# Performance work log

Measured on AMD Instinct MI355X. Metric: run time of the kernel, lower is better.

The kernel has to match this reference:

```python
import jax, jax.numpy as jnp
import numpy as np

BETA = 0.25


def setup_inputs() -> dict:
    key = jax.random.key(0)
    k1, k2 = jax.random.split(key)
    z = jax.random.normal(k1, (16, 64, 64, 64), dtype=jnp.float32)        # [B, e_dim, H, W]
    codebook = jax.random.normal(k2, (2048, 64), dtype=jnp.float32)       # [n_e, e_dim]
    return {"z": z, "codebook": codebook}


def reference(z, codebook):
    B, C, H, W = z.shape
    n_e = codebook.shape[0]
    sg = jax.lax.stop_gradient

    zp = jnp.transpose(z, (0, 2, 3, 1))                # [B, H, W, C]
    zf = zp.reshape(-1, C)                             # [N, C]

    # nearest-code logits (inner product; CE in source is dead code)
    logits = zf @ codebook.T                           # [N, n_e]
    idx = jnp.argmax(logits, axis=1)                   # [N]

    z_q = codebook[idx].reshape(zp.shape)              # [B, H, W, C]

    # commitment + codebook loss (this overwrites the CE loss in the source)
    loss = BETA * jnp.mean((sg(z_q) - zp) ** 2) + jnp.mean((z_q - sg(zp)) ** 2)

    # straight-through estimator
    z_q_st = zp + sg(z_q - zp)

    # perplexity via one-hot mean (scatter-add instead of dense one-hot)
    counts = jnp.zeros((n_e,), dtype=zp.dtype).at[idx].add(1.0)
    e_mean = counts / idx.shape[0]
    perplexity = jnp.exp(-jnp.sum(e_mean * jnp.log(e_mean + 1e-10)))

    indices = idx.reshape(B, H * W).astype(jnp.int32)
    z_q_out = jnp.transpose(z_q_st, (0, 3, 1, 2))      # back to [B, C, H, W]
    return z_q_out, loss, perplexity, indices
```

## Files before the change

### kernel.cpp

```cpp
#include <hip/hip_runtime.h>

#define C_DIM   64
#define HW      4096
#define NROWS   65536
#define N_E     2048
#define N_ELEM  4194304
#define OUT_LOSS_OFF 4194304
#define OUT_PPL_OFF  4194305
#define OUT_IDX_OFF  4194306

#define ROWS_B   128
#define NBLOCKS  (NROWS / ROWS_B)
#define NTILE    (N_E / 16)
#define TILE_U   384

typedef __attribute__((ext_vector_type(8))) short bf16x8;
typedef __attribute__((ext_vector_type(4))) float f32x4;

__device__ __forceinline__ unsigned short f2bf(float f) {
    unsigned u = __float_as_uint(f);
    return (unsigned short)((u + 0x7FFFu + ((u >> 16) & 1u)) >> 16);
}
__device__ __forceinline__ float bf2f(unsigned short b) {
    return __uint_as_float(((unsigned)b) << 16);
}

__global__ __launch_bounds__(256) void vq_prep(
    const float* __restrict__ cb, unsigned short* __restrict__ cbp,
    int* __restrict__ counts, float* __restrict__ loss_accum,
    int* __restrict__ done)
{
    const int u = blockIdx.x * 256 + threadIdx.x;
    if (u < N_E) counts[u] = 0;
    if (u == 0)  { *loss_accum = 0.f; *done = 0; }

    const int lane = u & 63;
    const int k2   = (u >> 6) & 1;
    const int tile = u >> 7;
    const int c    = tile * 16 + (lane & 15);
    const int k0   = k2 * 32 + (lane >> 4) * 8;

    const float4 va = *(const float4*)(cb + (size_t)c * C_DIM + k0);
    const float4 vb = *(const float4*)(cb + (size_t)c * C_DIM + k0 + 4);
    const float v[8] = {va.x, va.y, va.z, va.w, vb.x, vb.y, vb.z, vb.w};

    bf16x8 s1v, s2v, s3v;
#pragma unroll
    for (int i = 0; i < 8; ++i) {
        const unsigned short s1 = f2bf(v[i]);
        const float r1 = v[i] - bf2f(s1);
        const unsigned short s2 = f2bf(r1);
        const float r2 = r1 - bf2f(s2);
        s1v[i] = (short)s1;
        s2v[i] = (short)s2;
        s3v[i] = (short)f2bf(r2);
    }
    const size_t base = ((size_t)(tile * 3 + 0) * 2 + k2) * 512 + (size_t)lane * 8;
    *(bf16x8*)(cbp + base)        = s1v;
    *(bf16x8*)(cbp + base + 1024) = s2v;
    *(bf16x8*)(cbp + base + 2048) = s3v;
}

#define M16(A_, B_, C_) __builtin_amdgcn_mfma_f32_16x16x32_bf16((A_), (B_), (C_), 0, 0, 0)

#define PASS8(AA, ACC, NT)                                                      \
    ACC = M16(AA[0], zf[0][NT][0], ACC); ACC = M16(AA[1], zf[0][NT][1], ACC);   \
    ACC = M16(AA[0], zf[1][NT][0], ACC); ACC = M16(AA[1], zf[1][NT][1], ACC);   \
    ACC = M16(AA[2], zf[0][NT][0], ACC); ACC = M16(AA[3], zf[0][NT][1], ACC);   \
    ACC = M16(AA[2], zf[1][NT][0], ACC); ACC = M16(AA[3], zf[1][NT][1], ACC);   \
    ACC = M16(AA[0], zf[2][NT][0], ACC); ACC = M16(AA[1], zf[2][NT][1], ACC);   \
    ACC = M16(AA[4], zf[0][NT][0], ACC); ACC = M16(AA[5], zf[0][NT][1], ACC);   \
    ACC = M16(AA[2], zf[2][NT][0], ACC); ACC = M16(AA[3], zf[2][NT][1], ACC);   \
    ACC = M16(AA[4], zf[1][NT][0], ACC); ACC = M16(AA[5], zf[1][NT][1], ACC);

#define COMPUTE_TILE(T_, AA)                                                    \
    {                                                                           \
        f32x4 acc0 = zero4, acc1 = zero4;                                       \
        PASS8(AA, acc0, 0)                                                      \
        PASS8(AA, acc1, 1)                                                      \
        const int cbase = (T_) * 16 + lg * 4;                                   \
        _Pragma("unroll")                                                       \
        for (int r = 0; r < 4; ++r) {                                           \
            if (acc0[r] > best0) { best0 = acc0[r]; bi0 = cbase + r; }          \
            if (acc1[r] > best1) { best1 = acc1[r]; bi1 = cbase + r; }          \
        }                                                                       \
    }

#define LOADA(AA, T_)                                                           \
    {                                                                           \
        const bf16x8* p_ = cbpf + (size_t)(T_) * TILE_U;                        \
        _Pragma("unroll")                                                       \
        for (int f = 0; f < 6; ++f) AA[f] = p_[f * 64 + lane];                  \
    }

__global__ __launch_bounds__(256, 2) void vq_mfma(
    const float* __restrict__ z, const float* __restrict__ cb,
    const unsigned short* __restrict__ cbp, float* __restrict__ out,
    int* __restrict__ counts, float* __restrict__ loss_accum,
    int* __restrict__ done)
{
    __shared__ int   sidx[ROWS_B];
    __shared__ float wsum[4];
    __shared__ int   slast;

    const int tid  = threadIdx.x;
    const int lane = tid & 63;
    const int wv   = tid >> 6;
    const int l15  = lane & 15, lg = lane >> 4;
    const int row0 = blockIdx.x * ROWS_B;
    const int b    = row0 >> 12;
    const int hw0  = row0 & 4095;
    const float* zb = z + (size_t)b * C_DIM * HW + hw0;

    if (tid == 0) slast = 0;

    bf16x8 zf[3][2][2];
#pragma unroll
    for (int nt = 0; nt < 2; ++nt) {
        const int row_l = wv * 32 + nt * 16 + l15;
#pragma unroll
        for (int k2 = 0; k2 < 2; ++k2) {
#pragma unroll
            for (int i = 0; i < 8; ++i) {
                float v = zb[(size_t)(k2 * 32 + lg * 8 + i) * HW + row_l];
                unsigned short s1 = f2bf(v);
                float r1 = v - bf2f(s1);
                unsigned short s2 = f2bf(r1);
                float r2 = r1 - bf2f(s2);
                zf[0][nt][k2][i] = (short)s1;
                zf[1][nt][k2][i] = (short)s2;
                zf[2][nt][k2][i] = (short)f2bf(r2);
            }
        }
    }

    const bf16x8* cbpf = (const bf16x8*)cbp;
    float best0 = -3.4e38f, best1 = -3.4e38f;
    int   bi0 = 0, bi1 = 0;
    const f32x4 zero4 = {0.f, 0.f, 0.f, 0.f};

    bf16x8 A0[6], A1[6], A2[6], A3[6];
    LOADA(A0, 0) LOADA(A1, 1) LOADA(A2, 2)

#pragma unroll 1
    for (int t = 0; t < NTILE; t += 4) {
        const int p3 = t + 3;
        const int p4 = (t + 4 < NTILE) ? t + 4 : NTILE - 1;
        const int p5 = (t + 5 < NTILE) ? t + 5 : NTILE - 1;
        const int p6 = (t + 6 < NTILE) ? t + 6 : NTILE - 1;
        LOADA(A3, p3) COMPUTE_TILE(t,     A0)
        LOADA(A0, p4) COMPUTE_TILE(t + 1, A1)
        LOADA(A1, p5) COMPUTE_TILE(t + 2, A2)
        LOADA(A2, p6) COMPUTE_TILE(t + 3, A3)
    }

#pragma unroll
    for (int off = 16; off <= 32; off <<= 1) {
        float ob; int oi;
        ob = __shfl_xor(best0, off, 64); oi = __shfl_xor(bi0, off, 64);
        if (ob > best0 || (ob == best0 && oi < bi0)) { best0 = ob; bi0 = oi; }
        ob = __shfl_xor(best1, off, 64); oi = __shfl_xor(bi1, off, 64);
        if (ob > best1 || (ob == best1 && oi < bi1)) { best1 = ob; bi1 = oi; }
    }
    if (lane < 32) {
        const int nt = lane >> 4;
        const int row_l = wv * 32 + lane;
        const int ii = (nt == 0) ? bi0 : bi1;
        sidx[row_l] = ii;
        out[OUT_IDX_OFF + row0 + row_l] = (float)ii;
        atomicAdd(&counts[ii], 1);
    }
    __syncthreads();

    float* ob0 = out + (size_t)b * C_DIM * HW + hw0;
    float lsum = 0.f;
#pragma unroll
    for (int j = 0; j < 8; ++j) {
        const int m = j * 256 + tid;
        const int r = m & 127, c4 = m >> 7;
        const float4 q4 = *(const float4*)(cb + (size_t)sidx[r] * C_DIM + c4 * 4);
#pragma unroll
        for (int q = 0; q < 4; ++q) {
            const int c = c4 * 4 + q;
            const float zv = zb[(size_t)c * HW + r];
            const float qv = (q == 0) ? q4.x : (q == 1) ? q4.y : (q == 2) ? q4.z : q4.w;
            const float d = qv - zv;
            lsum += d * d;
            ob0[(size_t)c * HW + r] = zv + d;
        }
    }
    for (int off = 32; off > 0; off >>= 1) lsum += __shfl_down(lsum, off, 64);
    if (lane == 0) wsum[wv] = lsum;
    __syncthreads();

    if (tid == 0) {
        atomicAdd(loss_accum, wsum[0] + wsum[1] + wsum[2] + wsum[3]);
        __threadfence();
        const int tk = atomicAdd(done, 1);
        if (tk == NBLOCKS - 1) slast = 1;
    }
    __syncthreads();
    if (slast) {
        __threadfence();
        float h = 0.f;
        for (int e = tid; e < N_E; e += 256) {
            const int cnt = atomicAdd(&counts[e], 0);
            const float em = (float)cnt * (1.0f / (float)NROWS);
            h -= em * logf(em + 1e-10f);
        }
        for (int off = 32; off > 0; off >>= 1) h += __shfl_down(h, off, 64);
        if (lane == 0) wsum[wv] = h;
        __syncthreads();
        if (tid == 0) {
            const float H = wsum[0] + wsum[1] + wsum[2] + wsum[3];
            const float L = atomicAdd(loss_accum, 0.f);
            const float m = L * (1.0f / (float)N_ELEM);
            out[OUT_LOSS_OFF] = 0.25f * m + m;
            out[OUT_PPL_OFF]  = expf(H);
        }
    }
}

extern "C" void kernel_launch(void* const* d_in, const int* in_sizes, int n_in,
                              void* d_out, int out_size, void* d_ws, size_t ws_size,
                              hipStream_t stream)
{
    const float* z  = (const float*)d_in[0];
    const float* cb = (const float*)d_in[1];
    float* out = (float*)d_out;

    int*            counts     = (int*)d_ws;
    float*          loss_accum = (float*)((char*)d_ws + N_E * sizeof(int));
    int*            done       = (int*)((char*)d_ws + N_E * sizeof(int) + 4);
    unsigned short* cbp        = (unsigned short*)((char*)d_ws + 16384);

    vq_prep<<<64, 256, 0, stream>>>(cb, cbp, counts, loss_accum, done);
    vq_mfma<<<NBLOCKS, 256, 0, stream>>>(z, cb, cbp, out, counts, loss_accum, done);
}
```

Baseline: 188.1 us.

## Fuse codebook bf16 split into main kernel and replace prep kernel with memset

Removes the separate prep kernel that pre-split the codebook into three bf16 parts. The main kernel now loads raw fp32 codebook rows and does the three-way bf16 split inline, one tile ahead, with double buffering of raw loads instead of a four-deep prefetch of split fragments. Counters are zeroed with a memset. This drops one launch and the packed codebook traffic, but every block now repeats the split ALU work for all 2048 codes, which adds VALU work to the MFMA loop, and the prefetch distance is shorter.

New measurement: 242.2 us. 1.29x slower.

```diff
diff --git a/kernel.cpp b/kernel.cpp
--- a/kernel.cpp
+++ b/kernel.cpp
@@ -12,7 +12,6 @@
 #define ROWS_B   128
 #define NBLOCKS  (NROWS / ROWS_B)
 #define NTILE    (N_E / 16)
-#define TILE_U   384
 
 typedef __attribute__((ext_vector_type(8))) short bf16x8;
 typedef __attribute__((ext_vector_type(4))) float f32x4;
@@ -25,40 +24,22 @@
     return __uint_as_float(((unsigned)b) << 16);
 }
 
-__global__ __launch_bounds__(256) void vq_prep(
-    const float* __restrict__ cb, unsigned short* __restrict__ cbp,
-    int* __restrict__ counts, float* __restrict__ loss_accum,
-    int* __restrict__ done)
+__device__ __forceinline__ void split8(const float4 a, const float4 b,
+                                       bf16x8* s1v, bf16x8* s2v, bf16x8* s3v)
 {
-    const int u = blockIdx.x * 256 + threadIdx.x;
-    if (u < N_E) counts[u] = 0;
-    if (u == 0)  { *loss_accum = 0.f; *done = 0; }
-
-    const int lane = u & 63;
-    const int k2   = (u >> 6) & 1;
-    const int tile = u >> 7;
-    const int c    = tile * 16 + (lane & 15);
-    const int k0   = k2 * 32 + (lane >> 4) * 8;
-
-    const float4 va = *(const float4*)(cb + (size_t)c * C_DIM + k0);
-    const float4 vb = *(const float4*)(cb + (size_t)c * C_DIM + k0 + 4);
-    const float v[8] = {va.x, va.y, va.z, va.w, vb.x, vb.y, vb.z, vb.w};
-
-    bf16x8 s1v, s2v, s3v;
+    const float v[8] = {a.x, a.y, a.z, a.w, b.x, b.y, b.z, b.w};
+    bf16x8 t1, t2, t3;
 #pragma unroll
     for (int i = 0; i < 8; ++i) {
         const unsigned short s1 = f2bf(v[i]);
         const float r1 = v[i] - bf2f(s1);
         const unsigned short s2 = f2bf(r1);
         const float r2 = r1 - bf2f(s2);
-        s1v[i] = (short)s1;
-        s2v[i] = (short)s2;
-        s3v[i] = (short)f2bf(r2);
-    }
-    const size_t base = ((size_t)(tile * 3 + 0) * 2 + k2) * 512 + (size_t)lane * 8;
-    *(bf16x8*)(cbp + base)        = s1v;
-    *(bf16x8*)(cbp + base + 1024) = s2v;
-    *(bf16x8*)(cbp + base + 2048) = s3v;
+        t1[i] = (short)s1;
+        t2[i] = (short)s2;
+        t3[i] = (short)f2bf(r2);
+    }
+    *s1v = t1; *s2v = t2; *s3v = t3;
 }
 
 #define M16(A_, B_, C_) __builtin_amdgcn_mfma_f32_16x16x32_bf16((A_), (B_), (C_), 0, 0, 0)
@@ -73,11 +54,23 @@
     ACC = M16(AA[2], zf[2][NT][0], ACC); ACC = M16(AA[3], zf[2][NT][1], ACC);   \
     ACC = M16(AA[4], zf[1][NT][0], ACC); ACC = M16(AA[5], zf[1][NT][1], ACC);
 
-#define COMPUTE_TILE(T_, AA)                                                    \
+#define LOADRAW(R_, T_)                                                         \
     {                                                                           \
+        const float* p_ = cb + (size_t)((T_) * 16 + l15) * C_DIM + lg * 8;      \
+        R_[0] = *(const float4*)(p_);                                           \
+        R_[1] = *(const float4*)(p_ + 4);                                       \
+        R_[2] = *(const float4*)(p_ + 32);                                      \
+        R_[3] = *(const float4*)(p_ + 36);                                      \
+    }
+
+#define SPLIT_COMPUTE(T_, R_)                                                   \
+    {                                                                           \
+        bf16x8 A[6];                                                            \
+        split8(R_[0], R_[1], &A[0], &A[2], &A[4]);                              \
+        split8(R_[2], R_[3], &A[1], &A[3], &A[5]);                              \
         f32x4 acc0 = zero4, acc1 = zero4;                                       \
-        PASS8(AA, acc0, 0)                                                      \
-        PASS8(AA, acc1, 1)                                                      \
+        PASS8(A, acc0, 0)                                                       \
+        PASS8(A, acc1, 1)                                                       \
         const int cbase = (T_) * 16 + lg * 4;                                   \
         _Pragma("unroll")                                                       \
         for (int r = 0; r < 4; ++r) {                                           \
@@ -86,18 +79,10 @@
         }                                                                       \
     }
 
-#define LOADA(AA, T_)                                                           \
-    {                                                                           \
-        const bf16x8* p_ = cbpf + (size_t)(T_) * TILE_U;                        \
-        _Pragma("unroll")                                                       \
-        for (int f = 0; f < 6; ++f) AA[f] = p_[f * 64 + lane];                  \
-    }
-
 __global__ __launch_bounds__(256, 2) void vq_mfma(
     const float* __restrict__ z, const float* __restrict__ cb,
-    const unsigned short* __restrict__ cbp, float* __restrict__ out,
-    int* __restrict__ counts, float* __restrict__ loss_accum,
-    int* __restrict__ done)
+    float* __restrict__ out, int* __restrict__ counts,
+    float* __restrict__ loss_accum, int* __restrict__ done)
 {
     __shared__ int   sidx[ROWS_B];
     __shared__ float wsum[4];
@@ -134,24 +119,19 @@
         }
     }
 
-    const bf16x8* cbpf = (const bf16x8*)cbp;
     float best0 = -3.4e38f, best1 = -3.4e38f;
     int   bi0 = 0, bi1 = 0;
     const f32x4 zero4 = {0.f, 0.f, 0.f, 0.f};
 
-    bf16x8 A0[6], A1[6], A2[6], A3[6];
-    LOADA(A0, 0) LOADA(A1, 1) LOADA(A2, 2)
+    float4 Rc[4], Rn[4];
+    LOADRAW(Rc, 0)
 
 #pragma unroll 1
-    for (int t = 0; t < NTILE; t += 4) {
-        const int p3 = t + 3;
-        const int p4 = (t + 4 < NTILE) ? t + 4 : NTILE - 1;
-        const int p5 = (t + 5 < NTILE) ? t + 5 : NTILE - 1;
-        const int p6 = (t + 6 < NTILE) ? t + 6 : NTILE - 1;
-        LOADA(A3, p3) COMPUTE_TILE(t,     A0)
-        LOADA(A0, p4) COMPUTE_TILE(t + 1, A1)
-        LOADA(A1, p5) COMPUTE_TILE(t + 2, A2)
-        LOADA(A2, p6) COMPUTE_TILE(t + 3, A3)
+    for (int t = 0; t < NTILE; t += 2) {
+        LOADRAW(Rn, t + 1)
+        SPLIT_COMPUTE(t, Rc)
+        if (t + 2 < NTILE) LOADRAW(Rc, t + 2)
+        SPLIT_COMPUTE(t + 1, Rn)
     }
 
 #pragma unroll
@@ -229,11 +209,10 @@
     const float* cb = (const float*)d_in[1];
     float* out = (float*)d_out;
 
-    int*            counts     = (int*)d_ws;
-    float*          loss_accum = (float*)((char*)d_ws + N_E * sizeof(int));
-    int*            done       = (int*)((char*)d_ws + N_E * sizeof(int) + 4);
-    unsigned short* cbp        = (unsigned short*)((char*)d_ws + 16384);
-
-    vq_prep<<<64, 256, 0, stream>>>(cb, cbp, counts, loss_accum, done);
-    vq_mfma<<<NBLOCKS, 256, 0, stream>>>(z, cb, cbp, out, counts, loss_accum, done);
-}
+    int*   counts     = (int*)d_ws;
+    float* loss_accum = (float*)((char*)d_ws + N_E * sizeof(int));
+    int*   done       = (int*)((char*)d_ws + N_E * sizeof(int) + 4);
+
+    hipMemsetAsync(d_ws, 0, N_E * sizeof(int) + 8, stream);
+    vq_mfma<<<NBLOCKS, 256, 0, stream>>>(z, cb, out, counts, loss_accum, done);
+}
```

## Switch codebook matmul to 32x32x16 MFMA tiles with double-buffered loads

Applied to the files above, without the earlier changes.

Replaces the 16x16x32 bf16 MFMA tiling with 32x32x16 MFMAs over 32-code tiles. Each wave now covers 32 rows in one accumulator pair, and the codebook prep layout is changed to match. The 4-deep register prefetch ring becomes a 2-buffer ping-pong separated by sched_barriers, and the cross-lane argmax reduction shrinks to a single shuffle. The aim is fewer MFMA issues and fewer codebook fetches per row. The cost is higher register pressure from the 16-wide accumulators and 12-element A buffers, plus a shallower prefetch depth.

After: 207.4 us. 1.1x slower.

```diff
diff --git a/kernel.cpp b/kernel.cpp
--- a/kernel.cpp
+++ b/kernel.cpp
@@ -11,11 +11,11 @@
 
 #define ROWS_B   128
 #define NBLOCKS  (NROWS / ROWS_B)
-#define NTILE    (N_E / 16)
-#define TILE_U   384
-
-typedef __attribute__((ext_vector_type(8))) short bf16x8;
-typedef __attribute__((ext_vector_type(4))) float f32x4;
+#define NTILE32  (N_E / 32)
+#define TILE_U   768
+
+typedef __attribute__((ext_vector_type(8)))  short bf16x8;
+typedef __attribute__((ext_vector_type(16))) float f32x16;
 
 __device__ __forceinline__ unsigned short f2bf(float f) {
     unsigned u = __float_as_uint(f);
@@ -35,13 +35,13 @@
     if (u == 0)  { *loss_accum = 0.f; *done = 0; }
 
     const int lane = u & 63;
-    const int k2   = (u >> 6) & 1;
-    const int tile = u >> 7;
-    const int c    = tile * 16 + (lane & 15);
-    const int k0   = k2 * 32 + (lane >> 4) * 8;
-
-    const float4 va = *(const float4*)(cb + (size_t)c * C_DIM + k0);
-    const float4 vb = *(const float4*)(cb + (size_t)c * C_DIM + k0 + 4);
+    const int ks   = (u >> 6) & 3;
+    const int tile = u >> 8;
+    const int code = tile * 32 + (lane & 31);
+    const int k0   = ks * 16 + (lane >> 5) * 8;
+
+    const float4 va = *(const float4*)(cb + (size_t)code * C_DIM + k0);
+    const float4 vb = *(const float4*)(cb + (size_t)code * C_DIM + k0 + 4);
     const float v[8] = {va.x, va.y, va.z, va.w, vb.x, vb.y, vb.z, vb.w};
 
     bf16x8 s1v, s2v, s3v;
@@ -55,34 +55,30 @@
         s2v[i] = (short)s2;
         s3v[i] = (short)f2bf(r2);
     }
-    const size_t base = ((size_t)(tile * 3 + 0) * 2 + k2) * 512 + (size_t)lane * 8;
+    const size_t base = ((size_t)(tile * 3 + 0) * 4 + ks) * 512 + (size_t)lane * 8;
     *(bf16x8*)(cbp + base)        = s1v;
-    *(bf16x8*)(cbp + base + 1024) = s2v;
-    *(bf16x8*)(cbp + base + 2048) = s3v;
-}
-
-#define M16(A_, B_, C_) __builtin_amdgcn_mfma_f32_16x16x32_bf16((A_), (B_), (C_), 0, 0, 0)
-
-#define PASS8(AA, ACC, NT)                                                      \
-    ACC = M16(AA[0], zf[0][NT][0], ACC); ACC = M16(AA[1], zf[0][NT][1], ACC);   \
-    ACC = M16(AA[0], zf[1][NT][0], ACC); ACC = M16(AA[1], zf[1][NT][1], ACC);   \
-    ACC = M16(AA[2], zf[0][NT][0], ACC); ACC = M16(AA[3], zf[0][NT][1], ACC);   \
-    ACC = M16(AA[2], zf[1][NT][0], ACC); ACC = M16(AA[3], zf[1][NT][1], ACC);   \
-    ACC = M16(AA[0], zf[2][NT][0], ACC); ACC = M16(AA[1], zf[2][NT][1], ACC);   \
-    ACC = M16(AA[4], zf[0][NT][0], ACC); ACC = M16(AA[5], zf[0][NT][1], ACC);   \
-    ACC = M16(AA[2], zf[2][NT][0], ACC); ACC = M16(AA[3], zf[2][NT][1], ACC);   \
-    ACC = M16(AA[4], zf[1][NT][0], ACC); ACC = M16(AA[5], zf[1][NT][1], ACC);
-
-#define COMPUTE_TILE(T_, AA)                                                    \
+    *(bf16x8*)(cbp + base + 2048) = s2v;
+    *(bf16x8*)(cbp + base + 4096) = s3v;
+}
+
+#define M32(A_, B_, C_) __builtin_amdgcn_mfma_f32_32x32x16_bf16((A_), (B_), (C_), 0, 0, 0)
+
+#define P32(AA, SC, SZ)                                                         \
+    accA = M32(AA[(SC) * 4 + 0], zf[SZ][0], accA);                              \
+    accA = M32(AA[(SC) * 4 + 1], zf[SZ][1], accA);                              \
+    accB = M32(AA[(SC) * 4 + 2], zf[SZ][2], accB);                              \
+    accB = M32(AA[(SC) * 4 + 3], zf[SZ][3], accB);
+
+#define COMPUTE_TILE32(T_, AA)                                                  \
     {                                                                           \
-        f32x4 acc0 = zero4, acc1 = zero4;                                       \
-        PASS8(AA, acc0, 0)                                                      \
-        PASS8(AA, acc1, 1)                                                      \
-        const int cbase = (T_) * 16 + lg * 4;                                   \
+        f32x16 accA = zero16, accB = zero16;                                    \
+        P32(AA, 0, 0) P32(AA, 0, 1) P32(AA, 1, 0) P32(AA, 1, 1)                 \
+        P32(AA, 0, 2) P32(AA, 2, 0) P32(AA, 1, 2) P32(AA, 2, 1)                 \
         _Pragma("unroll")                                                       \
-        for (int r = 0; r < 4; ++r) {                                           \
-            if (acc0[r] > best0) { best0 = acc0[r]; bi0 = cbase + r; }          \
-            if (acc1[r] > best1) { best1 = acc1[r]; bi1 = cbase + r; }          \
+        for (int reg = 0; reg < 16; ++reg) {                                    \
+            const float v = accA[reg] + accB[reg];                              \
+            const int code = (T_) * 32 + (reg & 3) + 8 * (reg >> 2) + 4 * lh;   \
+            if (v > best) { best = v; bi = code; }                              \
         }                                                                       \
     }
 
@@ -90,7 +86,7 @@
     {                                                                           \
         const bf16x8* p_ = cbpf + (size_t)(T_) * TILE_U;                        \
         _Pragma("unroll")                                                       \
-        for (int f = 0; f < 6; ++f) AA[f] = p_[f * 64 + lane];                  \
+        for (int f = 0; f < 12; ++f) AA[f] = p_[f * 64 + lane];                 \
     }
 
 __global__ __launch_bounds__(256, 2) void vq_mfma(
@@ -106,7 +102,7 @@
     const int tid  = threadIdx.x;
     const int lane = tid & 63;
     const int wv   = tid >> 6;
-    const int l15  = lane & 15, lg = lane >> 4;
+    const int l31  = lane & 31, lh = lane >> 5;
     const int row0 = blockIdx.x * ROWS_B;
     const int b    = row0 >> 12;
     const int hw0  = row0 & 4095;
@@ -114,61 +110,53 @@
 
     if (tid == 0) slast = 0;
 
-    bf16x8 zf[3][2][2];
-#pragma unroll
-    for (int nt = 0; nt < 2; ++nt) {
-        const int row_l = wv * 32 + nt * 16 + l15;
-#pragma unroll
-        for (int k2 = 0; k2 < 2; ++k2) {
+    bf16x8 zf[3][4];
+    {
+        const int row_l = wv * 32 + l31;
+#pragma unroll
+        for (int ks = 0; ks < 4; ++ks) {
 #pragma unroll
             for (int i = 0; i < 8; ++i) {
-                float v = zb[(size_t)(k2 * 32 + lg * 8 + i) * HW + row_l];
+                float v = zb[(size_t)(ks * 16 + lh * 8 + i) * HW + row_l];
                 unsigned short s1 = f2bf(v);
                 float r1 = v - bf2f(s1);
                 unsigned short s2 = f2bf(r1);
                 float r2 = r1 - bf2f(s2);
-                zf[0][nt][k2][i] = (short)s1;
-                zf[1][nt][k2][i] = (short)s2;
-                zf[2][nt][k2][i] = (short)f2bf(r2);
+                zf[0][ks][i] = (short)s1;
+                zf[1][ks][i] = (short)s2;
+                zf[2][ks][i] = (short)f2bf(r2);
             }
         }
     }
 
     const bf16x8* cbpf = (const bf16x8*)cbp;
-    float best0 = -3.4e38f, best1 = -3.4e38f;
-    int   bi0 = 0, bi1 = 0;
-    const f32x4 zero4 = {0.f, 0.f, 0.f, 0.f};
-
-    bf16x8 A0[6], A1[6], A2[6], A3[6];
-    LOADA(A0, 0) LOADA(A1, 1) LOADA(A2, 2)
+    float best = -3.4e38f;
+    int   bi   = 0;
+    const f32x16 zero16 = {0,0,0,0,0,0,0,0,0,0,0,0,0,0,0,0};
+
+    bf16x8 Acur[12], Anxt[12];
+    LOADA(Acur, 0)
 
 #pragma unroll 1
-    for (int t = 0; t < NTILE; t += 4) {
-        const int p3 = t + 3;
-        const int p4 = (t + 4 < NTILE) ? t + 4 : NTILE - 1;
-        const int p5 = (t + 5 < NTILE) ? t + 5 : NTILE - 1;
-        const int p6 = (t + 6 < NTILE) ? t + 6 : NTILE - 1;
-        LOADA(A3, p3) COMPUTE_TILE(t,     A0)
-        LOADA(A0, p4) COMPUTE_TILE(t + 1, A1)
-        LOADA(A1, p5) COMPUTE_TILE(t + 2, A2)
-        LOADA(A2, p6) COMPUTE_TILE(t + 3, A3)
-    }
-
-#pragma unroll
-    for (int off = 16; off <= 32; off <<= 1) {
-        float ob; int oi;
-        ob = __shfl_xor(best0, off, 64); oi = __shfl_xor(bi0, off, 64);
-        if (ob > best0 || (ob == best0 && oi < bi0)) { best0 = ob; bi0 = oi; }
-        ob = __shfl_xor(best1, off, 64); oi = __shfl_xor(bi1, off, 64);
-        if (ob > best1 || (ob == best1 && oi < bi1)) { best1 = ob; bi1 = oi; }
+    for (int t = 0; t < NTILE32; t += 2) {
+        LOADA(Anxt, t + 1)
+        __builtin_amdgcn_sched_barrier(0);
+        COMPUTE_TILE32(t, Acur)
+        if (t + 2 < NTILE32) LOADA(Acur, t + 2)
+        __builtin_amdgcn_sched_barrier(0);
+        COMPUTE_TILE32(t + 1, Anxt)
+    }
+
+    {
+        const float ob = __shfl_xor(best, 32, 64);
+        const int   oi = __shfl_xor(bi, 32, 64);
+        if (ob > best || (ob == best && oi < bi)) { best = ob; bi = oi; }
     }
     if (lane < 32) {
-        const int nt = lane >> 4;
         const int row_l = wv * 32 + lane;
-        const int ii = (nt == 0) ? bi0 : bi1;
-        sidx[row_l] = ii;
-        out[OUT_IDX_OFF + row0 + row_l] = (float)ii;
-        atomicAdd(&counts[ii], 1);
+        sidx[row_l] = bi;
+        out[OUT_IDX_OFF + row0 + row_l] = (float)bi;
+        atomicAdd(&counts[bi], 1);
     }
     __syncthreads();
 
```

## Fuse codebook prep into main kernel via cooperative grid sync; shrink prefetch depth

Applied to the files above, without the earlier changes.

Removes the separate prep kernel. Each block of the main kernel now does a slice of the codebook split-to-bf16 conversion and zeroes its slice of the counters, then waits at a cooperative-groups grid sync before the MFMA search. This saves one kernel launch and the gap between the two kernels. To help all 512 blocks be co-resident, which a cooperative launch requires, the codebook prefetch drops from three tiles ahead to simple double buffering, using fewer registers. The cost is a grid-wide barrier and less latency hiding in the main loop.

Measured after the change: 257.5 us. 36.9% more time.

```diff
diff --git a/kernel.cpp b/kernel.cpp
--- a/kernel.cpp
+++ b/kernel.cpp
@@ -1,4 +1,7 @@
 #include <hip/hip_runtime.h>
+#include <hip/hip_cooperative_groups.h>
+
+namespace cg = cooperative_groups;
 
 #define C_DIM   64
 #define HW      4096
@@ -13,6 +16,7 @@
 #define NBLOCKS  (NROWS / ROWS_B)
 #define NTILE    (N_E / 16)
 #define TILE_U   384
+#define PREP_UNITS 16384
 
 typedef __attribute__((ext_vector_type(8))) short bf16x8;
 typedef __attribute__((ext_vector_type(4))) float f32x4;
@@ -23,42 +27,6 @@
 }
 __device__ __forceinline__ float bf2f(unsigned short b) {
     return __uint_as_float(((unsigned)b) << 16);
-}
-
-__global__ __launch_bounds__(256) void vq_prep(
-    const float* __restrict__ cb, unsigned short* __restrict__ cbp,
-    int* __restrict__ counts, float* __restrict__ loss_accum,
-    int* __restrict__ done)
-{
-    const int u = blockIdx.x * 256 + threadIdx.x;
-    if (u < N_E) counts[u] = 0;
-    if (u == 0)  { *loss_accum = 0.f; *done = 0; }
-
-    const int lane = u & 63;
-    const int k2   = (u >> 6) & 1;
-    const int tile = u >> 7;
-    const int c    = tile * 16 + (lane & 15);
-    const int k0   = k2 * 32 + (lane >> 4) * 8;
-
-    const float4 va = *(const float4*)(cb + (size_t)c * C_DIM + k0);
-    const float4 vb = *(const float4*)(cb + (size_t)c * C_DIM + k0 + 4);
-    const float v[8] = {va.x, va.y, va.z, va.w, vb.x, vb.y, vb.z, vb.w};
-
-    bf16x8 s1v, s2v, s3v;
-#pragma unroll
-    for (int i = 0; i < 8; ++i) {
-        const unsigned short s1 = f2bf(v[i]);
-        const float r1 = v[i] - bf2f(s1);
-        const unsigned short s2 = f2bf(r1);
-        const float r2 = r1 - bf2f(s2);
-        s1v[i] = (short)s1;
-        s2v[i] = (short)s2;
-        s3v[i] = (short)f2bf(r2);
-    }
-    const size_t base = ((size_t)(tile * 3 + 0) * 2 + k2) * 512 + (size_t)lane * 8;
-    *(bf16x8*)(cbp + base)        = s1v;
-    *(bf16x8*)(cbp + base + 1024) = s2v;
-    *(bf16x8*)(cbp + base + 2048) = s3v;
 }
 
 #define M16(A_, B_, C_) __builtin_amdgcn_mfma_f32_16x16x32_bf16((A_), (B_), (C_), 0, 0, 0)
@@ -93,9 +61,9 @@
         for (int f = 0; f < 6; ++f) AA[f] = p_[f * 64 + lane];                  \
     }
 
-__global__ __launch_bounds__(256, 2) void vq_mfma(
+__global__ __launch_bounds__(256, 2) void vq_all(
     const float* __restrict__ z, const float* __restrict__ cb,
-    const unsigned short* __restrict__ cbp, float* __restrict__ out,
+    unsigned short* __restrict__ cbp, float* __restrict__ out,
     int* __restrict__ counts, float* __restrict__ loss_accum,
     int* __restrict__ done)
 {
@@ -104,15 +72,51 @@
     __shared__ int   slast;
 
     const int tid  = threadIdx.x;
+    const int bid  = blockIdx.x;
     const int lane = tid & 63;
     const int wv   = tid >> 6;
     const int l15  = lane & 15, lg = lane >> 4;
-    const int row0 = blockIdx.x * ROWS_B;
+
+    if (tid == 0) slast = 0;
+
+    if (tid < PREP_UNITS / NBLOCKS) {
+        const int u    = bid * (PREP_UNITS / NBLOCKS) + tid;
+        const int pl   = u & 63;
+        const int k2   = (u >> 6) & 1;
+        const int tile = u >> 7;
+        const int c    = tile * 16 + (pl & 15);
+        const int k0   = k2 * 32 + (pl >> 4) * 8;
+
+        const float4 va = *(const float4*)(cb + (size_t)c * C_DIM + k0);
+        const float4 vb = *(const float4*)(cb + (size_t)c * C_DIM + k0 + 4);
+        const float v[8] = {va.x, va.y, va.z, va.w, vb.x, vb.y, vb.z, vb.w};
+
+        bf16x8 s1v, s2v, s3v;
+#pragma unroll
+        for (int i = 0; i < 8; ++i) {
+            const unsigned short s1 = f2bf(v[i]);
+            const float r1 = v[i] - bf2f(s1);
+            const unsigned short s2 = f2bf(r1);
+            const float r2 = r1 - bf2f(s2);
+            s1v[i] = (short)s1;
+            s2v[i] = (short)s2;
+            s3v[i] = (short)f2bf(r2);
+        }
+        const size_t base = ((size_t)(tile * 3 + 0) * 2 + k2) * 512 + (size_t)pl * 8;
+        *(bf16x8*)(cbp + base)        = s1v;
+        *(bf16x8*)(cbp + base + 1024) = s2v;
+        *(bf16x8*)(cbp + base + 2048) = s3v;
+    }
+    if (tid < N_E / NBLOCKS) counts[bid * (N_E / NBLOCKS) + tid] = 0;
+    if (bid == 0 && tid == 0) { *loss_accum = 0.f; *done = 0; }
+
+    __threadfence();
+    cg::this_grid().sync();
+
+    const int row0 = bid * ROWS_B;
     const int b    = row0 >> 12;
     const int hw0  = row0 & 4095;
     const float* zb = z + (size_t)b * C_DIM * HW + hw0;
-
-    if (tid == 0) slast = 0;
 
     bf16x8 zf[3][2][2];
 #pragma unroll
@@ -139,19 +143,15 @@
     int   bi0 = 0, bi1 = 0;
     const f32x4 zero4 = {0.f, 0.f, 0.f, 0.f};
 
-    bf16x8 A0[6], A1[6], A2[6], A3[6];
-    LOADA(A0, 0) LOADA(A1, 1) LOADA(A2, 2)
+    bf16x8 Acur[6], Anxt[6];
+    LOADA(Acur, 0)
 
 #pragma unroll 1
-    for (int t = 0; t < NTILE; t += 4) {
-        const int p3 = t + 3;
-        const int p4 = (t + 4 < NTILE) ? t + 4 : NTILE - 1;
-        const int p5 = (t + 5 < NTILE) ? t + 5 : NTILE - 1;
-        const int p6 = (t + 6 < NTILE) ? t + 6 : NTILE - 1;
-        LOADA(A3, p3) COMPUTE_TILE(t,     A0)
-        LOADA(A0, p4) COMPUTE_TILE(t + 1, A1)
-        LOADA(A1, p5) COMPUTE_TILE(t + 2, A2)
-        LOADA(A2, p6) COMPUTE_TILE(t + 3, A3)
+    for (int t = 0; t < NTILE; t += 2) {
+        LOADA(Anxt, t + 1)
+        COMPUTE_TILE(t, Acur)
+        if (t + 2 < NTILE) LOADA(Acur, t + 2)
+        COMPUTE_TILE(t + 1, Anxt)
     }
 
 #pragma unroll
@@ -234,6 +234,8 @@
     int*            done       = (int*)((char*)d_ws + N_E * sizeof(int) + 4);
     unsigned short* cbp        = (unsigned short*)((char*)d_ws + 16384);
 
-    vq_prep<<<64, 256, 0, stream>>>(cb, cbp, counts, loss_accum, done);
-    vq_mfma<<<NBLOCKS, 256, 0, stream>>>(z, cb, cbp, out, counts, loss_accum, done);
-}
+    void* args[] = {(void*)&z, (void*)&cb, (void*)&cbp, (void*)&out,
+                    (void*)&counts, (void*)&loss_accum, (void*)&done};
+    hipLaunchCooperativeKernel((const void*)vq_all, dim3(NBLOCKS), dim3(256),
+                               args, 0, stream);
+}
```
